# Optimization experiments

Hardware: AMD Instinct MI355X
Metric: run time of the kernel (lower is better)

## Reference

```python
import jax, jax.numpy as jnp
import numpy as np

N_TRAILS = 256
N_STEPS = 16
N_NODES = N_TRAILS * N_STEPS            # 4096
N_TRAIL_E = (N_STEPS - 1) * N_TRAILS    # 3840
N_DEV_E = N_STEPS * (N_TRAILS - 1)      # 4080
N_EDGES = N_TRAIL_E + N_DEV_E           # 7920


def setup_inputs() -> dict:
    key = jax.random.key(0)
    k1, k2, k3, k4, k5, k6 = jax.random.split(key, 6)
    nid = lambda i, t: i * N_TRAILS + t
    C = np.zeros((N_EDGES, N_NODES), np.float32)     # signed incidence for edge vectors (v - u)
    inc = np.zeros((N_EDGES, N_NODES), np.float32)   # per-node outgoing-direction signs
    dev_mask = np.zeros((N_EDGES,), np.float32)
    seq_edges = np.zeros((N_STEPS - 1, N_TRAILS), np.int32)
    e = 0
    for i in range(N_STEPS - 1):                      # trail edges
        for t in range(N_TRAILS):
            u, v = nid(i, t), nid(i + 1, t)
            C[e, u] = -1.0; C[e, v] = 1.0
            inc[e, u] = 1.0; inc[e, v] = -1.0
            seq_edges[i, t] = e
            e += 1
    for i in range(N_STEPS):                          # deviation edges within a step
        for t in range(N_TRAILS - 1):
            u, v = nid(i, t), nid(i, t + 1)
            C[e, u] = -1.0; C[e, v] = 1.0
            inc[e, u] = 1.0; inc[e, v] = -1.0
            dev_mask[e] = 1.0
            e += 1
    sequences = np.arange(N_NODES, dtype=np.int32).reshape(N_STEPS, N_TRAILS)
    lengths0 = jax.random.uniform(k3, (N_NODES, 1), jnp.float32) + 0.5
    keep = jax.random.bernoulli(k4, 0.5, (N_NODES, 1))
    lengths0 = jnp.where(keep, lengths0, 0.0)         # zeros trigger the plane-length path
    return {
        'xyz0': jax.random.normal(k1, (N_NODES, 3), jnp.float32),
        'loads': jax.random.normal(k2, (N_NODES, 3), jnp.float32) * 0.1,
        'lengths0': lengths0,
        'planes': jax.random.normal(k5, (N_NODES, 6), jnp.float32),
        'forces0': jax.random.normal(k6, (N_EDGES, 1), jnp.float32),
        'connectivity': jnp.asarray(C),
        'incidence': jnp.asarray(inc),
        'deviation_edges': jnp.asarray(dev_mask),
        'sequences': jnp.asarray(sequences),
        'sequences_edges': jnp.asarray(seq_edges),
    }


def _safe_normalize(v):
    s = jnp.sum(v * v, axis=-1, keepdims=True)
    return v * jax.lax.rsqrt(jnp.where(s == 0.0, 1.0, s))


def reference(xyz0, loads, lengths0, planes, forces0, connectivity, incidence,
              deviation_edges, sequences, sequences_edges):
    n_nodes = loads.shape[0]
    n_trails = sequences.shape[1]
    dev = deviation_edges[:, None]

    def step(carry, sequence):
        xyz, xyz_seq_in, residuals = carry
        xyz = xyz.at[sequence, :].set(xyz_seq_in)
        xyz_seq = xyz[sequence, :]                              # [S,3]
        padded = (sequence < 0)[:, None]
        # nodes_equilibrium: normalized edge vectors, deviation force balance
        vectors = _safe_normalize(connectivity @ xyz[:-1])      # [E,3]
        inc_seq = incidence[:, sequence] * dev                  # [E,S]
        f = forces0 * inc_seq                                   # [E,S]
        deviation = jnp.einsum('es,ed->sd', f, vectors)         # [S,3]
        res_new = residuals - deviation - loads[sequence, :]
        residuals = jnp.where(padded, residuals, res_new)
        # nodes_length_plane (vectorized node_length_plane)
        plane = planes[sequence, :]
        origin, normal = plane[:, :3], plane[:, 3:]
        zero_n = jnp.all(jnp.isclose(normal, 0.0), axis=-1, keepdims=True)
        normal = jnp.where(zero_n, 1.0, normal)
        cos_nop = jnp.where(zero_n[:, 0], 0.0, jnp.sum(normal * (origin - xyz_seq), axis=-1))
        zero_r = jnp.all(jnp.isclose(residuals, 0.0), axis=-1, keepdims=True)
        res_safe = jnp.where(zero_r, 1.0, residuals)
        denom = jnp.sum(normal * _safe_normalize(res_safe), axis=-1)
        len_plane = jnp.where(zero_r[:, 0], 0.0, cos_nop / denom)
        len_signed = lengths0[sequence].ravel()
        lengths_seq = jnp.where(len_signed != 0.0, len_signed, len_plane)
        # nodes_position
        xyz_next = xyz_seq + lengths_seq[:, None] * _safe_normalize(residuals)
        xyz_next = jnp.where(padded, xyz_seq, xyz_next)
        return (xyz, xyz_next, residuals), (residuals, lengths_seq)

    xyz = jnp.zeros((n_nodes + 1, 3), xyz0.dtype)               # extra row absorbs padded -1 writes
    carry0 = (xyz, xyz0[sequences[0], :], jnp.zeros((n_trails, 3), xyz0.dtype))
    (xyz, _, _), (res_all, len_all) = jax.lax.scan(step, carry0, sequences)
    xyz = xyz[:-1]
    reactions = jnp.zeros((n_nodes, 3), xyz.dtype).at[sequences[-1], :].set(res_all[-1])
    forces = jnp.where(forces0 != 0.0, forces0, 0.0)
    res_trail = res_all[:-1].reshape(-1, 3)
    len_trail = len_all[:-1].reshape(-1, 1)
    trail_forces = jnp.linalg.norm(res_trail, axis=-1, keepdims=True) * jnp.where(len_trail < 0.0, -1.0, 1.0)
    forces = forces.at[sequences_edges.ravel(), :].set(trail_forces)
    lengths = jnp.linalg.norm(connectivity @ xyz, axis=-1, keepdims=True)
    return xyz, reactions, lengths, loads, forces
```

## Files before the change

### kernel.cpp

```cpp
#include <hip/hip_runtime.h>

#define N_TRAILS 256
#define N_STEPS 16
#define N_NODES 4096
#define N_TRAIL_E 3840
#define N_DEV_E 4080
#define N_EDGES 7920

#define OFF_XYZ 0
#define OFF_REACT 12288
#define OFF_LEN 24576
#define OFF_LOADS 32496
#define OFF_FORCES 44784

__global__ __launch_bounds__(256, 1) void cem_fused(
    const float* __restrict__ xyz0,
    const float* __restrict__ loads,
    const float* __restrict__ lengths0,
    const float* __restrict__ planes,
    const float* __restrict__ forces0,
    float* __restrict__ out) {
    const int t = threadIdx.x;

    if (blockIdx.x != 0) {
        int idx = (blockIdx.x - 1) * 256 + t;
        if (idx < (N_TRAIL_E * 3)) out[OFF_REACT + idx] = 0.0f;
        if (idx < (N_NODES * 3)) out[OFF_LOADS + idx] = loads[idx];
        if (idx < N_DEV_E) out[OFF_FORCES + N_TRAIL_E + idx] = forces0[N_TRAIL_E + idx];
        return;
    }

    __shared__ float row[2][N_TRAILS * 3];

    float pl[N_STEPS][3];
    float pp[N_STEPS][6];
    float l0[N_STEPS];
    float fL[N_STEPS];
    float fR[N_STEPS];
#pragma unroll
    for (int i = 0; i < N_STEPS; ++i) {
        const int n = i * N_TRAILS + t;
        pl[i][0] = loads[3 * n + 0];
        pl[i][1] = loads[3 * n + 1];
        pl[i][2] = loads[3 * n + 2];
        const float2* p2 = (const float2*)(planes + 6 * n);
        float2 a = p2[0], b = p2[1], c = p2[2];
        pp[i][0] = a.x; pp[i][1] = a.y; pp[i][2] = b.x;
        pp[i][3] = b.y; pp[i][4] = c.x; pp[i][5] = c.y;
        l0[i] = lengths0[n];
        const int ebase = N_TRAIL_E + i * (N_TRAILS - 1);
        fL[i] = (t > 0) ? forces0[ebase + t - 1] : 0.0f;
        fR[i] = (t < N_TRAILS - 1) ? forces0[ebase + t] : 0.0f;
    }

    float px = xyz0[3 * t + 0];
    float py = xyz0[3 * t + 1];
    float pz = xyz0[3 * t + 2];
    float rx = 0.f, ry = 0.f, rz = 0.f;

#pragma unroll
    for (int i = 0; i < N_STEPS; ++i) {
        const int n = i * N_TRAILS + t;
        float* r = row[i & 1];

        out[OFF_XYZ + 3 * n + 0] = px;
        out[OFF_XYZ + 3 * n + 1] = py;
        out[OFF_XYZ + 3 * n + 2] = pz;
        r[3 * t + 0] = px;
        r[3 * t + 1] = py;
        r[3 * t + 2] = pz;
        __syncthreads();

        float dx = 0.f, dy = 0.f, dz = 0.f;
        if (t > 0) {
            float vx = px - r[3 * (t - 1) + 0];
            float vy = py - r[3 * (t - 1) + 1];
            float vz = pz - r[3 * (t - 1) + 2];
            float s = vx * vx + vy * vy + vz * vz;
            float inv = (s == 0.f) ? 1.f : (1.f / sqrtf(s));
            float f = fL[i];
            dx -= f * (vx * inv);
            dy -= f * (vy * inv);
            dz -= f * (vz * inv);
        }
        if (t < N_TRAILS - 1) {
            float vx = r[3 * (t + 1) + 0] - px;
            float vy = r[3 * (t + 1) + 1] - py;
            float vz = r[3 * (t + 1) + 2] - pz;
            float s = vx * vx + vy * vy + vz * vz;
            float inv = (s == 0.f) ? 1.f : (1.f / sqrtf(s));
            float f = fR[i];
            dx += f * (vx * inv);
            dy += f * (vy * inv);
            dz += f * (vz * inv);
            out[OFF_LEN + N_TRAIL_E + i * (N_TRAILS - 1) + t] = sqrtf(s);
        }

        rx = rx - dx - pl[i][0];
        ry = ry - dy - pl[i][1];
        rz = rz - dz - pl[i][2];

        float ox = pp[i][0], oy = pp[i][1], oz = pp[i][2];
        float nx = pp[i][3], ny = pp[i][4], nz = pp[i][5];
        bool zero_n = (fabsf(nx) <= 1e-8f) && (fabsf(ny) <= 1e-8f) && (fabsf(nz) <= 1e-8f);
        if (zero_n) { nx = 1.f; ny = 1.f; nz = 1.f; }
        float cos_nop = zero_n ? 0.f
                               : (nx * (ox - px) + ny * (oy - py) + nz * (oz - pz));
        bool zero_r = (fabsf(rx) <= 1e-8f) && (fabsf(ry) <= 1e-8f) && (fabsf(rz) <= 1e-8f);
        float rsx = zero_r ? 1.f : rx;
        float rsy = zero_r ? 1.f : ry;
        float rsz = zero_r ? 1.f : rz;
        float s2 = rsx * rsx + rsy * rsy + rsz * rsz;
        float inv2 = (s2 == 0.f) ? 1.f : (1.f / sqrtf(s2));
        float denom = nx * (rsx * inv2) + ny * (rsy * inv2) + nz * (rsz * inv2);
        float len_plane = zero_r ? 0.f : (cos_nop / denom);
        float l0v = l0[i];
        float L = (l0v != 0.f) ? l0v : len_plane;

        float sr = rx * rx + ry * ry + rz * rz;
        float rn = sqrtf(sr);
        if (i < N_STEPS - 1) {
            out[OFF_FORCES + i * N_TRAILS + t] = rn * ((L < 0.f) ? -1.f : 1.f);
            out[OFF_LEN + i * N_TRAILS + t] = (sr == 0.f) ? 0.f : fabsf(L);
        } else {
            out[OFF_REACT + 3 * n + 0] = rx;
            out[OFF_REACT + 3 * n + 1] = ry;
            out[OFF_REACT + 3 * n + 2] = rz;
        }

        float invr = (sr == 0.f) ? 1.f : (1.f / sqrtf(sr));
        px = px + L * (rx * invr);
        py = py + L * (ry * invr);
        pz = pz + L * (rz * invr);
    }
}

extern "C" void kernel_launch(void* const* d_in, const int* in_sizes, int n_in,
                              void* d_out, int out_size, void* d_ws, size_t ws_size,
                              hipStream_t stream) {
    const float* xyz0     = (const float*)d_in[0];
    const float* loads    = (const float*)d_in[1];
    const float* lengths0 = (const float*)d_in[2];
    const float* planes   = (const float*)d_in[3];
    const float* forces0  = (const float*)d_in[4];
    float* out = (float*)d_out;

    cem_fused<<<49, 256, 0, stream>>>(xyz0, loads, lengths0, planes, forces0, out);
}
```

Baseline: 19.65 us.

## Split sequential solve into halo wavefronts using shuffles instead of block barriers

Replaces the single 256-thread block, which synchronized every step through shared memory, with 8 single-wavefront blocks. Each block owns 32 trails plus 16-trail halos on both sides and exchanges neighbour positions with lane shuffles, so no barriers are needed. Halo lanes recompute neighbour state redundantly, and the halo width of 16 covers the 16-step dependency spread. This removes per-step __syncthreads and spreads the serial work across several CUs, at the cost of duplicated computation and more blocks for the copy work.

```diff
diff --git a/kernel.cpp b/kernel.cpp
--- a/kernel.cpp
+++ b/kernel.cpp
@@ -13,24 +13,29 @@
 #define OFF_LOADS 32496
 #define OFF_FORCES 44784
 
-__global__ __launch_bounds__(256, 1) void cem_fused(
+__global__ __launch_bounds__(64, 1) void cem_fused(
     const float* __restrict__ xyz0,
     const float* __restrict__ loads,
     const float* __restrict__ lengths0,
     const float* __restrict__ planes,
     const float* __restrict__ forces0,
     float* __restrict__ out) {
-    const int t = threadIdx.x;
+    const int lane = threadIdx.x;
+    const int b = blockIdx.x;
 
-    if (blockIdx.x != 0) {
-        int idx = (blockIdx.x - 1) * 256 + t;
+    if (b >= 8) {
+        int idx = (b - 8) * 64 + lane;
         if (idx < (N_TRAIL_E * 3)) out[OFF_REACT + idx] = 0.0f;
         if (idx < (N_NODES * 3)) out[OFF_LOADS + idx] = loads[idx];
         if (idx < N_DEV_E) out[OFF_FORCES + N_TRAIL_E + idx] = forces0[N_TRAIL_E + idx];
         return;
     }
 
-    __shared__ float row[2][N_TRAILS * 3];
+    const int tr_raw = 32 * b - 16 + lane;
+    const int tr = min(max(tr_raw, 0), N_TRAILS - 1);
+    const bool core = (lane >= 16) && (lane < 48);
+    const bool has_left = (tr_raw > 0);
+    const bool has_right = (tr_raw < N_TRAILS - 1);
 
     float pl[N_STEPS][3];
     float pp[N_STEPS][6];
@@ -39,43 +44,41 @@
     float fR[N_STEPS];
 #pragma unroll
     for (int i = 0; i < N_STEPS; ++i) {
-        const int n = i * N_TRAILS + t;
+        const int n = i * N_TRAILS + tr;
         pl[i][0] = loads[3 * n + 0];
         pl[i][1] = loads[3 * n + 1];
         pl[i][2] = loads[3 * n + 2];
         const float2* p2 = (const float2*)(planes + 6 * n);
-        float2 a = p2[0], b = p2[1], c = p2[2];
-        pp[i][0] = a.x; pp[i][1] = a.y; pp[i][2] = b.x;
-        pp[i][3] = b.y; pp[i][4] = c.x; pp[i][5] = c.y;
+        float2 a = p2[0], bb = p2[1], c = p2[2];
+        pp[i][0] = a.x;  pp[i][1] = a.y;  pp[i][2] = bb.x;
+        pp[i][3] = bb.y; pp[i][4] = c.x;  pp[i][5] = c.y;
         l0[i] = lengths0[n];
         const int ebase = N_TRAIL_E + i * (N_TRAILS - 1);
-        fL[i] = (t > 0) ? forces0[ebase + t - 1] : 0.0f;
-        fR[i] = (t < N_TRAILS - 1) ? forces0[ebase + t] : 0.0f;
+        fL[i] = forces0[ebase + max(tr - 1, 0)];
+        fR[i] = forces0[ebase + min(tr, N_TRAILS - 2)];
     }
 
-    float px = xyz0[3 * t + 0];
-    float py = xyz0[3 * t + 1];
-    float pz = xyz0[3 * t + 2];
+    float px = xyz0[3 * tr + 0];
+    float py = xyz0[3 * tr + 1];
+    float pz = xyz0[3 * tr + 2];
     float rx = 0.f, ry = 0.f, rz = 0.f;
 
 #pragma unroll
     for (int i = 0; i < N_STEPS; ++i) {
-        const int n = i * N_TRAILS + t;
-        float* r = row[i & 1];
+        const int n = i * N_TRAILS + tr_raw;
 
-        out[OFF_XYZ + 3 * n + 0] = px;
-        out[OFF_XYZ + 3 * n + 1] = py;
-        out[OFF_XYZ + 3 * n + 2] = pz;
-        r[3 * t + 0] = px;
-        r[3 * t + 1] = py;
-        r[3 * t + 2] = pz;
-        __syncthreads();
+        if (core) {
+            out[OFF_XYZ + 3 * n + 0] = px;
+            out[OFF_XYZ + 3 * n + 1] = py;
+            out[OFF_XYZ + 3 * n + 2] = pz;
+        }
+
+        float lx = __shfl(px, lane - 1), ly = __shfl(py, lane - 1), lz = __shfl(pz, lane - 1);
+        float qx = __shfl(px, lane + 1), qy = __shfl(py, lane + 1), qz = __shfl(pz, lane + 1);
 
         float dx = 0.f, dy = 0.f, dz = 0.f;
-        if (t > 0) {
-            float vx = px - r[3 * (t - 1) + 0];
-            float vy = py - r[3 * (t - 1) + 1];
-            float vz = pz - r[3 * (t - 1) + 2];
+        if (has_left) {
+            float vx = px - lx, vy = py - ly, vz = pz - lz;
             float s = vx * vx + vy * vy + vz * vz;
             float inv = (s == 0.f) ? 1.f : (1.f / sqrtf(s));
             float f = fL[i];
@@ -83,17 +86,15 @@
             dy -= f * (vy * inv);
             dz -= f * (vz * inv);
         }
-        if (t < N_TRAILS - 1) {
-            float vx = r[3 * (t + 1) + 0] - px;
-            float vy = r[3 * (t + 1) + 1] - py;
-            float vz = r[3 * (t + 1) + 2] - pz;
+        if (has_right) {
+            float vx = qx - px, vy = qy - py, vz = qz - pz;
             float s = vx * vx + vy * vy + vz * vz;
             float inv = (s == 0.f) ? 1.f : (1.f / sqrtf(s));
             float f = fR[i];
             dx += f * (vx * inv);
             dy += f * (vy * inv);
             dz += f * (vz * inv);
-            out[OFF_LEN + N_TRAIL_E + i * (N_TRAILS - 1) + t] = sqrtf(s);
+            if (core) out[OFF_LEN + N_TRAIL_E + i * (N_TRAILS - 1) + tr_raw] = sqrtf(s);
         }
 
         rx = rx - dx - pl[i][0];
@@ -120,9 +121,11 @@
         float sr = rx * rx + ry * ry + rz * rz;
         float rn = sqrtf(sr);
         if (i < N_STEPS - 1) {
-            out[OFF_FORCES + i * N_TRAILS + t] = rn * ((L < 0.f) ? -1.f : 1.f);
-            out[OFF_LEN + i * N_TRAILS + t] = (sr == 0.f) ? 0.f : fabsf(L);
-        } else {
+            if (core) {
+                out[OFF_FORCES + i * N_TRAILS + tr_raw] = rn * ((L < 0.f) ? -1.f : 1.f);
+                out[OFF_LEN + i * N_TRAILS + tr_raw] = (sr == 0.f) ? 0.f : fabsf(L);
+            }
+        } else if (core) {
             out[OFF_REACT + 3 * n + 0] = rx;
             out[OFF_REACT + 3 * n + 1] = ry;
             out[OFF_REACT + 3 * n + 2] = rz;
@@ -145,5 +148,5 @@
     const float* forces0  = (const float*)d_in[4];
     float* out = (float*)d_out;
 
-    cem_fused<<<49, 256, 0, stream>>>(xyz0, loads, lengths0, planes, forces0, out);
+    cem_fused<<<200, 64, 0, stream>>>(xyz0, loads, lengths0, planes, forces0, out);
 }
```

Measured after the change: 17.66 us. 1.11x faster.
